# Performance work log

Hardware: AMD Instinct MI355X
Metric: run time of the kernel (lower is better)

Reference implementation:

```python
import jax, jax.numpy as jnp
import numpy as np

N = 100000   # nodes
E = 1200000  # directed edges
F_IN, HID, EMB = 5, 64, 16

def setup_inputs() -> dict:
    key = jax.random.key(0)
    ks = jax.random.split(key, 12)
    # node features: [lambda, mu, is_comp, is_AND, is_OR]
    lam = jax.random.uniform(ks[0], (N, 1), jnp.float32) * 0.01
    mu = jax.random.uniform(ks[1], (N, 1), jnp.float32) * 0.1
    node_type = jax.random.randint(ks[2], (N,), 0, 3)
    onehot = jax.nn.one_hot(node_type, 3, dtype=jnp.float32)
    x = jnp.concatenate([lam, mu, onehot], axis=1)  # [N,5]
    edge_index = jax.random.randint(ks[3], (2, E), 0, N, dtype=jnp.int32)

    def lin(k, fi, fo):
        s = 1.0 / np.sqrt(fi)
        return jax.random.uniform(k, (fi, fo), jnp.float32, -s, s)

    return {
        "x": x, "edge_index": edge_index,
        "T": jnp.float32(100.0), "T_max": jnp.float32(500.0),
        "W1": lin(ks[4], F_IN, HID), "b1": jnp.zeros((HID,), jnp.float32),
        "W2": lin(ks[5], HID, HID), "b2": jnp.zeros((HID,), jnp.float32),
        "W3": lin(ks[6], HID, EMB), "b3": jnp.zeros((EMB,), jnp.float32),
        "P1": lin(ks[7], EMB + 8, 64), "pb1": jnp.zeros((64,), jnp.float32),
        "P2": lin(ks[8], 64, 32), "pb2": jnp.zeros((32,), jnp.float32),
        "P3": lin(ks[9], 32, 4), "pb3": jnp.zeros((4,), jnp.float32),
    }

def gcn_conv(h_in, src, dst, W, b):
    """PyG GCNConv: add self-loops, symmetric D^-1/2 (A+I) D^-1/2 norm."""
    h = h_in @ W  # [N,F]
    # degree with self-loops: 1 + in-degree (count on target nodes)
    deg = jax.ops.segment_sum(jnp.ones((E,), jnp.float32), dst, num_segments=N) + 1.0
    dinv = jax.lax.rsqrt(deg)  # [N]
    norm = dinv[src] * dinv[dst]  # [E]
    agg = jax.ops.segment_sum(h[src] * norm[:, None], dst, num_segments=N)
    agg = agg + h * (dinv * dinv)[:, None]  # self-loop term norm = 1/deg
    return agg + b

def reference(x, edge_index, T, T_max, W1, b1, W2, b2, W3, b3,
              P1, pb1, P2, pb2, P3, pb3):
    src, dst = edge_index[0], edge_index[1]
    h = jax.nn.relu(gcn_conv(x, src, dst, W1, b1))
    h = jax.nn.relu(gcn_conv(h, src, dst, W2, b2))
    h = gcn_conv(h, src, dst, W3, b3)
    embedding = jnp.mean(h, axis=0, keepdims=True)  # global_mean_pool, batch=0 -> [1,EMB]

    T_norm = T / T_max
    comp = x[:, 2]
    n_comp = jnp.sum(comp)
    n_AND = jnp.sum(x[:, 3])
    n_OR = jnp.sum(x[:, 4])
    safe = jnp.maximum(n_comp, 1.0)
    has = n_comp > 0
    avg_lambda = jnp.where(has, jnp.sum(x[:, 0] * comp) / safe, 0.0)
    avg_mu = jnp.where(has, jnp.sum(x[:, 1] * comp) / safe, 0.0)
    t_inv = 1.0 / (1.0 + T_norm)
    gf = jnp.stack([n_comp, n_AND, n_OR, n_AND + n_OR,
                    avg_lambda, avg_mu, T_norm * 50.0, t_inv * 50.0])[None, :]  # [1,8]

    emb = jnp.concatenate([embedding, gf], axis=1)  # [1,24]
    hmlp = jax.nn.relu(emb @ P1 + pb1)
    hmlp = jax.nn.relu(hmlp @ P2 + pb2)
    raw = hmlp @ P3 + pb3  # [1,4]

    val = jax.nn.softplus(raw + 2.0)
    alpha_min = 1.0 + val[:, 0]
    alpha_max = alpha_min + val[:, 1] + 0.5
    beta_min = 1.0 + val[:, 2]
    beta_max = beta_min + val[:, 3] + 0.5
    out = jnp.stack([alpha_min, alpha_max, beta_min, beta_max], axis=1)  # [1,4]
    return out, emb
```

## Files before the change

### kernel.cpp

```cpp
#include <hip/hip_runtime.h>

#define NN 100000
#define NE 1200000
#define NB_SCAN ((NN + 255) / 256)
#define NPASS 8
#define WNODES ((NN + NPASS - 1) / NPASS)
#define EB 128
#define GF_BLOCKS 64
#define P16_BLOCKS 1024

__global__ void k_hist(const int* __restrict__ ei, int* __restrict__ cnt) {
    int i = blockIdx.x * 256 + threadIdx.x;
    if (i < NE) atomicAdd(&cnt[ei[NE + i]], 1);
}

__global__ void k_scan_block(const int* __restrict__ cnt, int* __restrict__ incl,
                             int* __restrict__ bsum, float* __restrict__ dinv) {
    __shared__ int s[256];
    int t = threadIdx.x;
    int i = blockIdx.x * 256 + t;
    int v = (i < NN) ? cnt[i] : 0;
    if (i < NN) dinv[i] = rsqrtf((float)v + 1.0f);
    s[t] = v;
    __syncthreads();
    for (int off = 1; off < 256; off <<= 1) {
        int add = (t >= off) ? s[t - off] : 0;
        __syncthreads();
        s[t] += add;
        __syncthreads();
    }
    if (i < NN) incl[i] = s[t];
    if (t == 255) bsum[blockIdx.x] = s[255];
}

__global__ void k_scan_bsum(int* __restrict__ bsum) {
    __shared__ int s[512];
    int t = threadIdx.x;
    s[t] = (t < NB_SCAN) ? bsum[t] : 0;
    __syncthreads();
    for (int off = 1; off < 512; off <<= 1) {
        int add = (t >= off) ? s[t - off] : 0;
        __syncthreads();
        s[t] += add;
        __syncthreads();
    }
    if (t < NB_SCAN) bsum[t] = s[t];
}

__global__ void k_scan_add(const int* __restrict__ cnt, const int* __restrict__ incl,
                           const int* __restrict__ bsum, int* __restrict__ rowptr) {
    int i = blockIdx.x * 256 + threadIdx.x;
    if (i >= NN) return;
    int base = (blockIdx.x > 0) ? bsum[blockIdx.x - 1] : 0;
    rowptr[i] = base + incl[i] - cnt[i];
    if (i == 0) rowptr[NN] = NE;
}

__global__ void k_scatter_win(const int* __restrict__ ei, const int* __restrict__ rowptr,
                              int* __restrict__ cursor, int* __restrict__ srcs) {
    int pass = blockIdx.x & (NPASS - 1);
    int blk  = blockIdx.x / NPASS;
    int lo = pass * WNODES;
    int hi = lo + WNODES;
    for (int e = blk * 256 + threadIdx.x; e < NE; e += EB * 256) {
        int dst = ei[NE + e];
        if (dst >= lo && dst < hi) {
            int pos = rowptr[dst] + atomicAdd(&cursor[dst], 1);
            srcs[pos] = ei[e];
        }
    }
}

__global__ void k_aggx(const int* __restrict__ rowptr, const int* __restrict__ srcs,
                       const float* __restrict__ dinv, const float* __restrict__ x,
                       float* __restrict__ aggx) {
    int t = threadIdx.x;
    int n = blockIdx.x * 4 + (t >> 6);
    if (n >= NN) return;
    int lane = t & 63, c = lane & 7, slot = lane >> 3;
    int e0 = rowptr[n], e1 = rowptr[n + 1];
    float es = 0.f;
    if (c < 5) {
        for (int j = e0 + slot; j < e1; j += 8) {
            int s = srcs[j];
            es += x[(size_t)s * 5 + c] * dinv[s];
        }
    }
    es += __shfl_xor(es, 8, 64);
    es += __shfl_xor(es, 16, 64);
    es += __shfl_xor(es, 32, 64);
    float dvn = dinv[n];
    if (slot == 0 && c < 5)
        aggx[(size_t)n * 5 + c] = es * dvn + x[(size_t)n * 5 + c] * dvn * dvn;
}

__global__ void k_lin_first(const float* __restrict__ aggx, const float* __restrict__ W,
                            const float* __restrict__ b, float* __restrict__ h) {
    __shared__ float Ws[5 * 64];
    __shared__ float bs[64];
    int t = threadIdx.x;
    for (int i = t; i < 320; i += 256) Ws[i] = W[i];
    if (t < 64) bs[t] = b[t];
    __syncthreads();
    int r = t >> 6, c = t & 63;
    int row = blockIdx.x * 4 + r;
    if (row >= NN) return;
    float acc = bs[c];
#pragma unroll
    for (int k = 0; k < 5; k++) acc += aggx[(size_t)row * 5 + k] * Ws[k * 64 + c];
    h[(size_t)row * 64 + c] = fmaxf(acc, 0.f);
}

__global__ void k_lin64(const float* __restrict__ in, const float* __restrict__ W,
                        float* __restrict__ h) {
    __shared__ float Ws[64 * 64];
    __shared__ float rows[256];
    int t = threadIdx.x;
    for (int i = t; i < 4096; i += 256) Ws[i] = W[i];
    int base = blockIdx.x * 4;
    int gidx = base * 64 + t;
    rows[t] = (gidx < NN * 64) ? in[gidx] : 0.f;
    __syncthreads();
    int r = t >> 6, c = t & 63, row = base + r;
    if (row >= NN) return;
    float acc = 0.f;
#pragma unroll
    for (int k = 0; k < 64; k++) acc += rows[r * 64 + k] * Ws[k * 64 + c];
    h[(size_t)row * 64 + c] = acc;
}

__global__ void k_lin3(const float* __restrict__ in, const float* __restrict__ W,
                       float* __restrict__ h) {
    __shared__ float Ws[64 * 16];
    __shared__ float rows[16 * 64];
    int t = threadIdx.x;
    for (int i = t; i < 1024; i += 256) Ws[i] = W[i];
    int base = blockIdx.x * 16;
    for (int i = t; i < 1024; i += 256) {
        int g = base * 64 + i;
        rows[i] = (g < NN * 64) ? in[g] : 0.f;
    }
    __syncthreads();
    int r = t >> 4, c = t & 15, row = base + r;
    if (row >= NN) return;
    float acc = 0.f;
#pragma unroll
    for (int k = 0; k < 64; k++) acc += rows[r * 64 + k] * Ws[k * 16 + c];
    h[(size_t)row * 16 + c] = acc;
}

template <bool RELU>
__global__ void k_agg64(const int* __restrict__ rowptr, const int* __restrict__ srcs,
                        const float* __restrict__ dinv, const float* __restrict__ h,
                        const float* __restrict__ b, float* __restrict__ out) {
    int t = threadIdx.x;
    int n = blockIdx.x * 4 + (t >> 6);
    if (n >= NN) return;
    int c = t & 63;
    int e0 = rowptr[n], e1 = rowptr[n + 1];
    float dvn = dinv[n];
    float acc0 = 0.f, acc1 = 0.f, acc2 = 0.f, acc3 = 0.f;
    int j = e0;
    for (; j + 3 < e1; j += 4) {
        int s0 = srcs[j], s1 = srcs[j + 1], s2 = srcs[j + 2], s3 = srcs[j + 3];
        float w0 = dinv[s0], w1 = dinv[s1], w2 = dinv[s2], w3 = dinv[s3];
        acc0 += h[(size_t)s0 * 64 + c] * w0;
        acc1 += h[(size_t)s1 * 64 + c] * w1;
        acc2 += h[(size_t)s2 * 64 + c] * w2;
        acc3 += h[(size_t)s3 * 64 + c] * w3;
    }
    for (; j < e1; j++) {
        int s0 = srcs[j];
        acc0 += h[(size_t)s0 * 64 + c] * dinv[s0];
    }
    float v = ((acc0 + acc1) + (acc2 + acc3)) * dvn
            + h[(size_t)n * 64 + c] * dvn * dvn + b[c];
    if (RELU) v = fmaxf(v, 0.f);
    out[(size_t)n * 64 + c] = v;
}

__global__ void k_agg16_part(const int* __restrict__ rowptr, const int* __restrict__ srcs,
                             const float* __restrict__ dinv, const float* __restrict__ h,
                             const float* __restrict__ b, float* __restrict__ part16) {
    int t = threadIdx.x;
    int lane = t & 63, wv = t >> 6;
    int c = lane & 15, slot = lane >> 4;
    int gw = blockIdx.x * 4 + wv;
    int nw = gridDim.x * 4;
    float acc = 0.f;
    for (int n = gw; n < NN; n += nw) {
        int e0 = rowptr[n], e1 = rowptr[n + 1];
        float dvn = dinv[n];
        float es = 0.f;
        for (int j = e0 + slot; j < e1; j += 4) {
            int s0 = srcs[j];
            es += h[(size_t)s0 * 16 + c] * dinv[s0];
        }
        es += __shfl_xor(es, 16, 64);
        es += __shfl_xor(es, 32, 64);
        if (slot == 0)
            acc += es * dvn + h[(size_t)n * 16 + c] * dvn * dvn + b[c];
    }
    __shared__ float s[4][16];
    if (slot == 0) s[wv][c] = acc;
    __syncthreads();
    if (t < 16) part16[blockIdx.x * 16 + t] = (s[0][t] + s[1][t]) + (s[2][t] + s[3][t]);
}

__global__ void k_gf_part(const float* __restrict__ x, float* __restrict__ gfpart) {
    int t = threadIdx.x;
    float sc = 0, sa = 0, so = 0, sl = 0, sm = 0;
    for (int i = blockIdx.x * 256 + t; i < NN; i += gridDim.x * 256) {
        float lam = x[i * 5 + 0], mu = x[i * 5 + 1];
        float c = x[i * 5 + 2], a = x[i * 5 + 3], o = x[i * 5 + 4];
        sc += c; sa += a; so += o; sl += lam * c; sm += mu * c;
    }
    __shared__ float s[256];
    float vals[5] = {sc, sa, so, sl, sm};
#pragma unroll
    for (int k = 0; k < 5; k++) {
        s[t] = vals[k];
        __syncthreads();
        for (int off = 128; off > 0; off >>= 1) {
            if (t < off) s[t] += s[t + off];
            __syncthreads();
        }
        if (t == 0) gfpart[blockIdx.x * 5 + k] = s[0];
        __syncthreads();
    }
}

__device__ __forceinline__ float softplus_f(float x) {
    return (x > 20.f) ? x : log1pf(expf(x));
}

__global__ void k_mlp(const float* __restrict__ part16, const float* __restrict__ gfpart,
                      const float* __restrict__ T, const float* __restrict__ Tmax,
                      const float* __restrict__ P1, const float* __restrict__ pb1,
                      const float* __restrict__ P2, const float* __restrict__ pb2,
                      const float* __restrict__ P3, const float* __restrict__ pb3,
                      float* __restrict__ out) {
    __shared__ float s[256];
    __shared__ float emb[24];
    __shared__ float hm1[64];
    __shared__ float hm2[32];
    __shared__ float val[4];
    int t = threadIdx.x;
    {
        int c = t & 15, g = t >> 4;
        float acc = 0.f;
        for (int r = g; r < P16_BLOCKS; r += 16) acc += part16[r * 16 + c];
        s[t] = acc;
        __syncthreads();
        for (int off = 128; off >= 16; off >>= 1) {
            if (t < off) s[t] += s[t + off];
            __syncthreads();
        }
        if (t < 16) emb[t] = s[t] / (float)NN;
    }
    if (t < 5) {
        float acc = 0.f;
        for (int r = 0; r < GF_BLOCKS; r++) acc += gfpart[r * 5 + t];
        s[t] = acc;
    }
    __syncthreads();
    if (t == 0) {
        float sc = s[0], sa = s[1], so = s[2], sl = s[3], sm = s[4];
        float Tn = T[0] / Tmax[0];
        emb[16] = sc;
        emb[17] = sa;
        emb[18] = so;
        emb[19] = sa + so;
        float safe = fmaxf(sc, 1.0f);
        bool has = sc > 0.f;
        emb[20] = has ? sl / safe : 0.f;
        emb[21] = has ? sm / safe : 0.f;
        emb[22] = Tn * 50.f;
        emb[23] = (1.f / (1.f + Tn)) * 50.f;
    }
    __syncthreads();
    if (t < 64) {
        float acc = pb1[t];
#pragma unroll
        for (int k = 0; k < 24; k++) acc += emb[k] * P1[k * 64 + t];
        hm1[t] = fmaxf(acc, 0.f);
    }
    __syncthreads();
    if (t < 32) {
        float acc = pb2[t];
#pragma unroll
        for (int k = 0; k < 64; k++) acc += hm1[k] * P2[k * 32 + t];
        hm2[t] = fmaxf(acc, 0.f);
    }
    __syncthreads();
    if (t < 4) {
        float acc = pb3[t];
#pragma unroll
        for (int k = 0; k < 32; k++) acc += hm2[k] * P3[k * 4 + t];
        val[t] = softplus_f(acc + 2.0f);
    }
    __syncthreads();
    if (t == 0) {
        float amin = 1.f + val[0];
        float amax = amin + val[1] + 0.5f;
        float bmin = 1.f + val[2];
        float bmax = bmin + val[3] + 0.5f;
        out[0] = amin; out[1] = amax; out[2] = bmin; out[3] = bmax;
    }
    if (t >= 4 && t < 28) out[t] = emb[t - 4];
}

extern "C" void kernel_launch(void* const* d_in, const int* in_sizes, int n_in,
                              void* d_out, int out_size, void* d_ws, size_t ws_size,
                              hipStream_t stream) {
    const float* x    = (const float*)d_in[0];
    const int*   ei   = (const int*)d_in[1];
    const float* T    = (const float*)d_in[2];
    const float* Tmax = (const float*)d_in[3];
    const float* W1   = (const float*)d_in[4];
    const float* b1   = (const float*)d_in[5];
    const float* W2   = (const float*)d_in[6];
    const float* b2   = (const float*)d_in[7];
    const float* W3   = (const float*)d_in[8];
    const float* b3   = (const float*)d_in[9];
    const float* P1   = (const float*)d_in[10];
    const float* pb1  = (const float*)d_in[11];
    const float* P2   = (const float*)d_in[12];
    const float* pb2  = (const float*)d_in[13];
    const float* P3   = (const float*)d_in[14];
    const float* pb3  = (const float*)d_in[15];
    float* out = (float*)d_out;

    char* w = (char*)d_ws;
    float* bufH   = (float*)w;                 w += (size_t)NN * 64 * 4;
    float* bufA   = (float*)w;                 w += (size_t)NN * 64 * 4;
    int*   cnt    = (int*)w;                   w += (size_t)NN * 4;
    int*   cursor = (int*)w;                   w += (size_t)NN * 4;
    float* dinv   = (float*)w;                 w += (size_t)NN * 4;
    int*   incl   = (int*)w;                   w += (size_t)NN * 4;
    int*   rowptr = (int*)w;                   w += (size_t)(NN + 1) * 4;
    int*   srcs   = (int*)w;                   w += (size_t)NE * 4;
    int*   bsum   = (int*)w;                   w += 512 * 4;
    float* aggx   = (float*)w;                 w += (size_t)NN * 5 * 4;
    float* part16 = (float*)w;                 w += (size_t)P16_BLOCKS * 16 * 4;
    float* gfpart = (float*)w;                 w += (size_t)GF_BLOCKS * 5 * 4;

    hipMemsetAsync(cnt, 0, 2 * (size_t)NN * sizeof(int), stream);

    k_hist<<<(NE + 255) / 256, 256, 0, stream>>>(ei, cnt);
    k_scan_block<<<NB_SCAN, 256, 0, stream>>>(cnt, incl, bsum, dinv);
    k_scan_bsum<<<1, 512, 0, stream>>>(bsum);
    k_scan_add<<<NB_SCAN, 256, 0, stream>>>(cnt, incl, bsum, rowptr);
    k_scatter_win<<<NPASS * EB, 256, 0, stream>>>(ei, rowptr, cursor, srcs);

    k_aggx<<<(NN + 3) / 4, 256, 0, stream>>>(rowptr, srcs, dinv, x, aggx);
    k_lin_first<<<(NN + 3) / 4, 256, 0, stream>>>(aggx, W1, b1, bufA);

    k_lin64<<<(NN + 3) / 4, 256, 0, stream>>>(bufA, W2, bufH);
    k_agg64<true><<<(NN + 3) / 4, 256, 0, stream>>>(rowptr, srcs, dinv, bufH, b2, bufA);

    k_lin3<<<(NN + 15) / 16, 256, 0, stream>>>(bufA, W3, bufH);
    k_agg16_part<<<P16_BLOCKS, 256, 0, stream>>>(rowptr, srcs, dinv, bufH, b3, part16);

    k_gf_part<<<GF_BLOCKS, 256, 0, stream>>>(x, gfpart);
    k_mlp<<<1, 256, 0, stream>>>(part16, gfpart, T, Tmax, P1, pb1, P2, pb2, P3, pb3, out);
}
```

Before: 470.4 us.

## Collapse final GCN layer into weighted column sum and pack edge weights

```diff
diff --git a/kernel.cpp b/kernel.cpp
--- a/kernel.cpp
+++ b/kernel.cpp
@@ -7,7 +7,7 @@
 #define WNODES ((NN + NPASS - 1) / NPASS)
 #define EB 128
 #define GF_BLOCKS 64
-#define P16_BLOCKS 1024
+#define WS_BLOCKS 1024
 
 __global__ void k_hist(const int* __restrict__ ei, int* __restrict__ cnt) {
     int i = blockIdx.x * 256 + threadIdx.x;
@@ -57,7 +57,8 @@
 }
 
 __global__ void k_scatter_win(const int* __restrict__ ei, const int* __restrict__ rowptr,
-                              int* __restrict__ cursor, int* __restrict__ srcs) {
+                              int* __restrict__ cursor, int2* __restrict__ sw,
+                              const float* __restrict__ dinv, float* __restrict__ colw) {
     int pass = blockIdx.x & (NPASS - 1);
     int blk  = blockIdx.x / NPASS;
     int lo = pass * WNODES;
@@ -65,13 +66,15 @@
     for (int e = blk * 256 + threadIdx.x; e < NE; e += EB * 256) {
         int dst = ei[NE + e];
         if (dst >= lo && dst < hi) {
+            int src = ei[e];
             int pos = rowptr[dst] + atomicAdd(&cursor[dst], 1);
-            srcs[pos] = ei[e];
+            sw[pos] = make_int2(src, __float_as_int(dinv[src]));
+            atomicAdd(&colw[src], dinv[dst]);
         }
     }
 }
 
-__global__ void k_aggx(const int* __restrict__ rowptr, const int* __restrict__ srcs,
+__global__ void k_aggx(const int* __restrict__ rowptr, const int2* __restrict__ sw,
                        const float* __restrict__ dinv, const float* __restrict__ x,
                        float* __restrict__ aggx) {
     int t = threadIdx.x;
@@ -82,8 +85,8 @@
     float es = 0.f;
     if (c < 5) {
         for (int j = e0 + slot; j < e1; j += 8) {
-            int s = srcs[j];
-            es += x[(size_t)s * 5 + c] * dinv[s];
+            int2 p = sw[j];
+            es += x[(size_t)p.x * 5 + c] * __int_as_float(p.y);
         }
     }
     es += __shfl_xor(es, 8, 64);
@@ -129,28 +132,8 @@
     h[(size_t)row * 64 + c] = acc;
 }
 
-__global__ void k_lin3(const float* __restrict__ in, const float* __restrict__ W,
-                       float* __restrict__ h) {
-    __shared__ float Ws[64 * 16];
-    __shared__ float rows[16 * 64];
-    int t = threadIdx.x;
-    for (int i = t; i < 1024; i += 256) Ws[i] = W[i];
-    int base = blockIdx.x * 16;
-    for (int i = t; i < 1024; i += 256) {
-        int g = base * 64 + i;
-        rows[i] = (g < NN * 64) ? in[g] : 0.f;
-    }
-    __syncthreads();
-    int r = t >> 4, c = t & 15, row = base + r;
-    if (row >= NN) return;
-    float acc = 0.f;
-#pragma unroll
-    for (int k = 0; k < 64; k++) acc += rows[r * 64 + k] * Ws[k * 16 + c];
-    h[(size_t)row * 16 + c] = acc;
-}
-
 template <bool RELU>
-__global__ void k_agg64(const int* __restrict__ rowptr, const int* __restrict__ srcs,
+__global__ void k_agg64(const int* __restrict__ rowptr, const int2* __restrict__ sw,
                         const float* __restrict__ dinv, const float* __restrict__ h,
                         const float* __restrict__ b, float* __restrict__ out) {
     int t = threadIdx.x;
@@ -162,16 +145,15 @@
     float acc0 = 0.f, acc1 = 0.f, acc2 = 0.f, acc3 = 0.f;
     int j = e0;
     for (; j + 3 < e1; j += 4) {
-        int s0 = srcs[j], s1 = srcs[j + 1], s2 = srcs[j + 2], s3 = srcs[j + 3];
-        float w0 = dinv[s0], w1 = dinv[s1], w2 = dinv[s2], w3 = dinv[s3];
-        acc0 += h[(size_t)s0 * 64 + c] * w0;
-        acc1 += h[(size_t)s1 * 64 + c] * w1;
-        acc2 += h[(size_t)s2 * 64 + c] * w2;
-        acc3 += h[(size_t)s3 * 64 + c] * w3;
+        int2 p0 = sw[j], p1 = sw[j + 1], p2 = sw[j + 2], p3 = sw[j + 3];
+        acc0 += h[(size_t)p0.x * 64 + c] * __int_as_float(p0.y);
+        acc1 += h[(size_t)p1.x * 64 + c] * __int_as_float(p1.y);
+        acc2 += h[(size_t)p2.x * 64 + c] * __int_as_float(p2.y);
+        acc3 += h[(size_t)p3.x * 64 + c] * __int_as_float(p3.y);
     }
     for (; j < e1; j++) {
-        int s0 = srcs[j];
-        acc0 += h[(size_t)s0 * 64 + c] * dinv[s0];
+        int2 p0 = sw[j];
+        acc0 += h[(size_t)p0.x * 64 + c] * __int_as_float(p0.y);
     }
     float v = ((acc0 + acc1) + (acc2 + acc3)) * dvn
             + h[(size_t)n * 64 + c] * dvn * dvn + b[c];
@@ -179,32 +161,21 @@
     out[(size_t)n * 64 + c] = v;
 }
 
-__global__ void k_agg16_part(const int* __restrict__ rowptr, const int* __restrict__ srcs,
-                             const float* __restrict__ dinv, const float* __restrict__ h,
-                             const float* __restrict__ b, float* __restrict__ part16) {
-    int t = threadIdx.x;
-    int lane = t & 63, wv = t >> 6;
-    int c = lane & 15, slot = lane >> 4;
-    int gw = blockIdx.x * 4 + wv;
-    int nw = gridDim.x * 4;
+__global__ void k_wsum(const float* __restrict__ h2, const float* __restrict__ colw,
+                       const float* __restrict__ dinv, float* __restrict__ part) {
+    int t = threadIdx.x;
+    int c = t & 63;
     float acc = 0.f;
-    for (int n = gw; n < NN; n += nw) {
-        int e0 = rowptr[n], e1 = rowptr[n + 1];
-        float dvn = dinv[n];
-        float es = 0.f;
-        for (int j = e0 + slot; j < e1; j += 4) {
-            int s0 = srcs[j];
-            es += h[(size_t)s0 * 16 + c] * dinv[s0];
-        }
-        es += __shfl_xor(es, 16, 64);
-        es += __shfl_xor(es, 32, 64);
-        if (slot == 0)
-            acc += es * dvn + h[(size_t)n * 16 + c] * dvn * dvn + b[c];
-    }
-    __shared__ float s[4][16];
-    if (slot == 0) s[wv][c] = acc;
-    __syncthreads();
-    if (t < 16) part16[blockIdx.x * 16 + t] = (s[0][t] + s[1][t]) + (s[2][t] + s[3][t]);
+    for (int r = blockIdx.x * 4 + (t >> 6); r < NN; r += WS_BLOCKS * 4) {
+        float dv = dinv[r];
+        acc += dv * (colw[r] + dv) * h2[(size_t)r * 64 + c];
+    }
+    __shared__ float s[256];
+    s[t] = acc;
+    __syncthreads();
+    if (t < 128) s[t] += s[t + 128];
+    __syncthreads();
+    if (t < 64) part[blockIdx.x * 64 + t] = s[t] + s[t + 64];
 }
 
 __global__ void k_gf_part(const float* __restrict__ x, float* __restrict__ gfpart) {
@@ -234,34 +205,42 @@
     return (x > 20.f) ? x : log1pf(expf(x));
 }
 
-__global__ void k_mlp(const float* __restrict__ part16, const float* __restrict__ gfpart,
+__global__ void k_mlp(const float* __restrict__ part64, const float* __restrict__ gfpart,
+                      const float* __restrict__ W3, const float* __restrict__ b3,
                       const float* __restrict__ T, const float* __restrict__ Tmax,
                       const float* __restrict__ P1, const float* __restrict__ pb1,
                       const float* __restrict__ P2, const float* __restrict__ pb2,
                       const float* __restrict__ P3, const float* __restrict__ pb3,
                       float* __restrict__ out) {
     __shared__ float s[256];
+    __shared__ float m[64];
     __shared__ float emb[24];
     __shared__ float hm1[64];
     __shared__ float hm2[32];
     __shared__ float val[4];
     int t = threadIdx.x;
     {
-        int c = t & 15, g = t >> 4;
+        int c = t & 63, g = t >> 6;
         float acc = 0.f;
-        for (int r = g; r < P16_BLOCKS; r += 16) acc += part16[r * 16 + c];
+        for (int r = g; r < WS_BLOCKS; r += 4) acc += part64[r * 64 + c];
         s[t] = acc;
         __syncthreads();
-        for (int off = 128; off >= 16; off >>= 1) {
-            if (t < off) s[t] += s[t + off];
-            __syncthreads();
-        }
-        if (t < 16) emb[t] = s[t] / (float)NN;
-    }
-    if (t < 5) {
+        if (t < 128) s[t] += s[t + 128];
+        __syncthreads();
+        if (t < 64) m[t] = s[t] + s[t + 64];
+        __syncthreads();
+    }
+    if (t < 16) {
         float acc = 0.f;
-        for (int r = 0; r < GF_BLOCKS; r++) acc += gfpart[r * 5 + t];
-        s[t] = acc;
+#pragma unroll
+        for (int c = 0; c < 64; c++) acc += m[c] * W3[c * 16 + t];
+        emb[t] = acc / (float)NN + b3[t];
+    }
+    if (t >= 32 && t < 37) {
+        int k = t - 32;
+        float acc = 0.f;
+        for (int r = 0; r < GF_BLOCKS; r++) acc += gfpart[r * 5 + k];
+        s[k] = acc;
     }
     __syncthreads();
     if (t == 0) {
@@ -336,32 +315,34 @@
     float* bufA   = (float*)w;                 w += (size_t)NN * 64 * 4;
     int*   cnt    = (int*)w;                   w += (size_t)NN * 4;
     int*   cursor = (int*)w;                   w += (size_t)NN * 4;
+    float* colw   = (float*)w;                 w += (size_t)NN * 4;
     float* dinv   = (float*)w;                 w += (size_t)NN * 4;
     int*   incl   = (int*)w;                   w += (size_t)NN * 4;
     int*   rowptr = (int*)w;                   w += (size_t)(NN + 1) * 4;
-    int*   srcs   = (int*)w;                   w += (size_t)NE * 4;
+    w = (char*)(((size_t)w + 15) & ~(size_t)15);
+    int2*  sw     = (int2*)w;                  w += (size_t)NE * 8;
     int*   bsum   = (int*)w;                   w += 512 * 4;
     float* aggx   = (float*)w;                 w += (size_t)NN * 5 * 4;
-    float* part16 = (float*)w;                 w += (size_t)P16_BLOCKS * 16 * 4;
+    float* part64 = (float*)w;                 w += (size_t)WS_BLOCKS * 64 * 4;
     float* gfpart = (float*)w;                 w += (size_t)GF_BLOCKS * 5 * 4;
 
-    hipMemsetAsync(cnt, 0, 2 * (size_t)NN * sizeof(int), stream);
+    hipMemsetAsync(cnt, 0, 3 * (size_t)NN * sizeof(int), stream);
 
     k_hist<<<(NE + 255) / 256, 256, 0, stream>>>(ei, cnt);
     k_scan_block<<<NB_SCAN, 256, 0, stream>>>(cnt, incl, bsum, dinv);
     k_scan_bsum<<<1, 512, 0, stream>>>(bsum);
     k_scan_add<<<NB_SCAN, 256, 0, stream>>>(cnt, incl, bsum, rowptr);
-    k_scatter_win<<<NPASS * EB, 256, 0, stream>>>(ei, rowptr, cursor, srcs);
-
-    k_aggx<<<(NN + 3) / 4, 256, 0, stream>>>(rowptr, srcs, dinv, x, aggx);
+    k_scatter_win<<<NPASS * EB, 256, 0, stream>>>(ei, rowptr, cursor, sw, dinv, colw);
+
+    k_aggx<<<(NN + 3) / 4, 256, 0, stream>>>(rowptr, sw, dinv, x, aggx);
     k_lin_first<<<(NN + 3) / 4, 256, 0, stream>>>(aggx, W1, b1, bufA);
 
     k_lin64<<<(NN + 3) / 4, 256, 0, stream>>>(bufA, W2, bufH);
-    k_agg64<true><<<(NN + 3) / 4, 256, 0, stream>>>(rowptr, srcs, dinv, bufH, b2, bufA);
-
-    k_lin3<<<(NN + 15) / 16, 256, 0, stream>>>(bufA, W3, bufH);
-    k_agg16_part<<<P16_BLOCKS, 256, 0, stream>>>(rowptr, srcs, dinv, bufH, b3, part16);
+    k_agg64<true><<<(NN + 3) / 4, 256, 0, stream>>>(rowptr, sw, dinv, bufH, b2, bufA);
+
+    k_wsum<<<WS_BLOCKS, 256, 0, stream>>>(bufA, colw, dinv, part64);
 
     k_gf_part<<<GF_BLOCKS, 256, 0, stream>>>(x, gfpart);
-    k_mlp<<<1, 256, 0, stream>>>(part16, gfpart, T, Tmax, P1, pb1, P2, pb2, P3, pb3, out);
-}
+    k_mlp<<<1, 256, 0, stream>>>(part64, gfpart, W3, b3, T, Tmax,
+                                 P1, pb1, P2, pb2, P3, pb3, out);
+}
```

Measured after the change: 502.2 us. 1.07x slower.
